# Kernel optimization log

Measured on AMD Instinct MI355X. Metric: run time of the kernel, lower is better.

## Reference

```python
import jax, jax.numpy as jnp
import numpy as np

N_QUBITS = 4
N_FEATURES = 16
B = 1048576


def _bcast(theta):
    # theta: scalar or [B]; make broadcastable against [B,2,2,2] amp slices
    return theta if jnp.ndim(theta) == 0 else theta.reshape(theta.shape[0], 1, 1, 1)


def apply_ry(state, theta, w):
    # state: [B,2,2,2,2] complex; RY(theta) on wire w
    th = _bcast(theta)
    c = jnp.cos(th / 2).astype(state.dtype)
    s = jnp.sin(th / 2).astype(state.dtype)
    st = jnp.moveaxis(state, w + 1, -1)
    a0, a1 = st[..., 0], st[..., 1]
    st = jnp.stack([c * a0 - s * a1, s * a0 + c * a1], axis=-1)
    return jnp.moveaxis(st, -1, w + 1)


def apply_rz(state, theta, w):
    # RZ(theta) = diag(e^{-i theta/2}, e^{+i theta/2}) on wire w
    th = _bcast(theta)
    ph = jnp.exp(-0.5j * th.astype(jnp.float32)).astype(state.dtype)
    st = jnp.moveaxis(state, w + 1, -1)
    a0, a1 = st[..., 0], st[..., 1]
    st = jnp.stack([ph * a0, jnp.conj(ph) * a1], axis=-1)
    return jnp.moveaxis(st, -1, w + 1)


def cnot(state, c, t):
    st = jnp.moveaxis(state, (c + 1, t + 1), (-2, -1))  # [...,2(ctrl),2(tgt)]
    st = jnp.stack([st[..., 0, :], st[..., 1, ::-1]], axis=-2)
    return jnp.moveaxis(st, (-2, -1), (c + 1, t + 1))


def quantum_encoder_batched(x, qw):
    # x: [B,16] float32, qw: [8] float32 -> latents [B,4] (PauliZ expvals)
    b = x.shape[0]
    state = jnp.zeros((b, 16), jnp.complex64).at[:, 0].set(1.0)
    state = state.reshape(b, 2, 2, 2, 2)
    pi = jnp.float32(np.pi)
    for i in range(N_QUBITS):
        state = apply_ry(state, x[:, i] * pi, i)
        state = apply_rz(state, x[:, i + N_QUBITS] * pi, i)
    for i in range(N_QUBITS - 1):
        state = cnot(state, i, i + 1)
    for i in range(N_QUBITS):
        state = apply_ry(state, qw[2 * i], i)
        state = apply_rz(state, qw[2 * i + 1], i)
    for i in range(N_QUBITS - 1):
        state = cnot(state, i, i + 1)
    probs = state.real ** 2 + state.imag ** 2  # [B,2,2,2,2]
    zs = []
    for i in range(N_QUBITS):
        axes = tuple(a for a in range(1, N_QUBITS + 1) if a != i + 1)
        p = probs.sum(axes)  # [B,2]
        zs.append(p[:, 0] - p[:, 1])
    return jnp.stack(zs, axis=1)  # [B,4]


def setup_inputs() -> dict:
    key = jax.random.key(0)
    ks = jax.random.split(key, 8)
    x = jax.random.uniform(ks[0], (B, N_FEATURES), dtype=jnp.float32)
    q_weights = 0.01 * jax.random.normal(ks[1], (2 * N_QUBITS,), dtype=jnp.float32)
    # decoder: Linear(4,16) -> ReLU -> Linear(16,32) -> ReLU -> Linear(32,16)
    W1 = jax.random.normal(ks[2], (16, 4), dtype=jnp.float32) / jnp.sqrt(4.0)
    b1 = jnp.zeros((16,), jnp.float32)
    W2 = jax.random.normal(ks[3], (32, 16), dtype=jnp.float32) / jnp.sqrt(16.0)
    b2 = jnp.zeros((32,), jnp.float32)
    W3 = jax.random.normal(ks[4], (16, 32), dtype=jnp.float32) / jnp.sqrt(32.0)
    b3 = jnp.zeros((16,), jnp.float32)
    return {"x": x, "q_weights": q_weights, "W1": W1, "b1": b1,
            "W2": W2, "b2": b2, "W3": W3, "b3": b3}


def reference(x, q_weights, W1, b1, W2, b2, W3, b3):
    z = quantum_encoder_batched(x, q_weights)          # [B,4]
    h = jax.nn.relu(z @ W1.T + b1)                      # [B,16]
    h = jax.nn.relu(h @ W2.T + b2)                      # [B,32]
    return h @ W3.T + b3                                # [B,16]
```

## Files before the change

kernel.cpp:

```cpp
#include <hip/hip_runtime.h>
#include <math.h>

using u32 = unsigned int;
typedef float v2f __attribute__((ext_vector_type(2)));

__device__ __forceinline__ v2f pkfma(v2f a, v2f b, v2f c) {
    return __builtin_elementwise_fma(a, b, c);
}
__device__ __forceinline__ v2f s2(float x) { return (v2f){x, x}; }

#define WS_FLOATS 1160

__global__ void cvt_weights_kernel(
    const float* __restrict__ qw, const float* __restrict__ W1, const float* __restrict__ b1,
    const float* __restrict__ W2, const float* __restrict__ b2, const float* __restrict__ W3,
    const float* __restrict__ b3, float* __restrict__ o)
{
    int t = blockIdx.x * blockDim.x + threadIdx.x;
    if (t >= WS_FLOATS) return;
    float v;
    if (t < 64) {
        int k = t >> 4, j = t & 15;
        v = W1[j * 4 + k];
    } else if (t < 80) {
        v = b1[t - 64];
    } else if (t < 592) {
        int idx = t - 80, k = idx >> 5, j = idx & 31;
        v = W2[j * 16 + k];
    } else if (t < 624) {
        v = b2[t - 592];
    } else if (t < 1136) {
        int idx = t - 624, k = idx >> 4, j = idx & 15;
        v = W3[j * 32 + k];
    } else if (t < 1152) {
        v = b3[t - 1136];
    } else if (t < 1156) {
        v = cosf(qw[2 * (t - 1152)] * 0.5f);
    } else {
        v = sinf(qw[2 * (t - 1156)] * 0.5f);
    }
    o[t] = v;
}

template<bool WS>
__global__ void __launch_bounds__(256) qae_main(
    const float* __restrict__ x,
    const float* __restrict__ wf,
    const float* __restrict__ qwp,
    const float* __restrict__ W1p, const float* __restrict__ b1p,
    const float* __restrict__ W2p, const float* __restrict__ b2p,
    const float* __restrict__ W3p, const float* __restrict__ b3p,
    float* __restrict__ outv, int n)
{
    int b = blockIdx.x * blockDim.x + threadIdx.x;
    if (b >= n) return;

    auto T1v = [&](int k, int j) -> v2f {
        if (WS) { int o = k * 16 + 2 * j; return (v2f){wf[o], wf[o + 1]}; }
        return (v2f){W1p[(2 * j) * 4 + k], W1p[(2 * j + 1) * 4 + k]};
    };
    auto T2v = [&](int k, int j) -> v2f {
        if (WS) { int o = 80 + k * 32 + 2 * j; return (v2f){wf[o], wf[o + 1]}; }
        return (v2f){W2p[(2 * j) * 16 + k], W2p[(2 * j + 1) * 16 + k]};
    };
    auto T3v = [&](int k, int j) -> v2f {
        if (WS) { int o = 624 + k * 16 + 2 * j; return (v2f){wf[o], wf[o + 1]}; }
        return (v2f){W3p[(2 * j) * 32 + k], W3p[(2 * j + 1) * 32 + k]};
    };
    auto B1v = [&](int j) -> v2f {
        if (WS) return (v2f){wf[64 + 2 * j], wf[64 + 2 * j + 1]};
        return (v2f){b1p[2 * j], b1p[2 * j + 1]};
    };
    auto B2v = [&](int j) -> v2f {
        if (WS) return (v2f){wf[592 + 2 * j], wf[592 + 2 * j + 1]};
        return (v2f){b2p[2 * j], b2p[2 * j + 1]};
    };
    auto B3v = [&](int j) -> v2f {
        if (WS) return (v2f){wf[1136 + 2 * j], wf[1136 + 2 * j + 1]};
        return (v2f){b3p[2 * j], b3p[2 * j + 1]};
    };

    const float4* xf = reinterpret_cast<const float4*>(x);
    float4 xa = xf[(size_t)b * 4];
    float4 xc = xf[(size_t)b * 4 + 1];
    float th[4] = { xa.x, xa.y, xa.z, xa.w };
    float ph[4] = { xc.x, xc.y, xc.z, xc.w };

    float u0r[4], u0i[4], u1r[4], u1i[4];
    #pragma unroll
    for (int i = 0; i < 4; ++i) {
        float ct = __builtin_amdgcn_cosf(th[i] * 0.25f);
        float st = __builtin_amdgcn_sinf(th[i] * 0.25f);
        float cp = __builtin_amdgcn_cosf(ph[i] * 0.25f);
        float sp = __builtin_amdgcn_sinf(ph[i] * 0.25f);
        u0r[i] = ct * cp;  u0i[i] = -ct * sp;
        u1r[i] = st * cp;  u1i[i] = st * sp;
    }

    float p01r[4], p01i[4], p23r[4], p23i[4];
    #pragma unroll
    for (int a = 0; a < 2; ++a) {
        #pragma unroll
        for (int c = 0; c < 2; ++c) {
            float arq = a ? u1r[0] : u0r[0], aiq = a ? u1i[0] : u0i[0];
            float brq = c ? u1r[1] : u0r[1], biq = c ? u1i[1] : u0i[1];
            p01r[a*2+c] = arq*brq - aiq*biq;
            p01i[a*2+c] = arq*biq + aiq*brq;
            float crq = a ? u1r[2] : u0r[2], ciq = a ? u1i[2] : u0i[2];
            float drq = c ? u1r[3] : u0r[3], diq = c ? u1i[3] : u0i[3];
            p23r[a*2+c] = crq*drq - ciq*diq;
            p23i[a*2+c] = crq*diq + ciq*drq;
        }
    }

    v2f amp[16];
    #pragma unroll
    for (int i = 0; i < 16; ++i) {
        int q0 = (i>>3)&1, q1 = (i>>2)&1, q2 = (i>>1)&1, q3 = i&1;
        int g = (q0<<3) | ((q1^q0)<<2) | ((q2^q1)<<1) | (q3^q2);
        int hi = g >> 2, lo = g & 3;
        amp[i] = (v2f){ p01r[hi]*p23r[lo] - p01i[hi]*p23i[lo],
                        p01r[hi]*p23i[lo] + p01i[hi]*p23r[lo] };
    }

    #pragma unroll
    for (int w = 0; w < 4; ++w) {
        float c, s;
        if (WS) { c = wf[1152 + w]; s = wf[1156 + w]; }
        else {
            const float INV4PI = 0.07957747154594767f;
            c = __builtin_amdgcn_cosf(qwp[2*w] * INV4PI);
            s = __builtin_amdgcn_sinf(qwp[2*w] * INV4PI);
        }
        v2f vc = s2(c), vs = s2(s);
        int stride = 1 << (3 - w);
        #pragma unroll
        for (int m = 0; m < 16; ++m) {
            if (m & stride) continue;
            int i0 = m, i1 = m | stride;
            v2f a0 = amp[i0], a1 = amp[i1];
            amp[i0] = pkfma(vc, a0, -(vs * a1));
            amp[i1] = pkfma(vc, a1,  (vs * a0));
        }
    }

    float p[16];
    #pragma unroll
    for (int i = 0; i < 16; ++i) {
        int q0 = (i>>3)&1, q1 = (i>>2)&1, q2 = (i>>1)&1, q3 = i&1;
        int g = (q0<<3) | ((q1^q0)<<2) | ((q2^q1)<<1) | (q3^q2);
        v2f q = amp[g] * amp[g];
        p[i] = q.x + q.y;
    }

    float s2a[8], s4[4];
    #pragma unroll
    for (int j = 0; j < 8; ++j) s2a[j] = p[2*j] + p[2*j+1];
    #pragma unroll
    for (int j = 0; j < 4; ++j) s4[j] = s2a[2*j] + s2a[2*j+1];
    float z0 = (s4[0] + s4[1]) - (s4[2] + s4[3]);
    float z1 = (s4[0] - s4[1]) + (s4[2] - s4[3]);
    float z2 = (s2a[0] - s2a[1]) + (s2a[2] - s2a[3]) + (s2a[4] - s2a[5]) + (s2a[6] - s2a[7]);
    float z3 = (p[0]-p[1]) + (p[2]-p[3]) + (p[4]-p[5]) + (p[6]-p[7])
             + (p[8]-p[9]) + (p[10]-p[11]) + (p[12]-p[13]) + (p[14]-p[15]);
    float zv[4] = { z0, z1, z2, z3 };

    const v2f vzero = s2(0.f);

    v2f acc1[8];
    #pragma unroll
    for (int j = 0; j < 8; ++j) acc1[j] = B1v(j);
    #pragma unroll
    for (int k = 0; k < 4; ++k) {
        v2f zk = s2(zv[k]);
        #pragma unroll
        for (int j = 0; j < 8; ++j) acc1[j] = pkfma(T1v(k, j), zk, acc1[j]);
    }
    float h1[16];
    #pragma unroll
    for (int j = 0; j < 8; ++j) {
        v2f r = __builtin_elementwise_max(acc1[j], vzero);
        h1[2*j] = r.x; h1[2*j+1] = r.y;
    }

    v2f acc2[16];
    #pragma unroll
    for (int j = 0; j < 16; ++j) acc2[j] = B2v(j);
    #pragma unroll
    for (int k = 0; k < 16; ++k) {
        v2f hk = s2(h1[k]);
        #pragma unroll
        for (int j = 0; j < 16; ++j) acc2[j] = pkfma(T2v(k, j), hk, acc2[j]);
    }
    float h2[32];
    #pragma unroll
    for (int j = 0; j < 16; ++j) {
        v2f r = __builtin_elementwise_max(acc2[j], vzero);
        h2[2*j] = r.x; h2[2*j+1] = r.y;
    }

    v2f acc3[8];
    #pragma unroll
    for (int j = 0; j < 8; ++j) acc3[j] = B3v(j);
    #pragma unroll
    for (int k = 0; k < 32; ++k) {
        v2f hk = s2(h2[k]);
        #pragma unroll
        for (int j = 0; j < 8; ++j) acc3[j] = pkfma(T3v(k, j), hk, acc3[j]);
    }

    float4* op = reinterpret_cast<float4*>(outv) + (size_t)b * 4;
    op[0] = make_float4(acc3[0].x, acc3[0].y, acc3[1].x, acc3[1].y);
    op[1] = make_float4(acc3[2].x, acc3[2].y, acc3[3].x, acc3[3].y);
    op[2] = make_float4(acc3[4].x, acc3[4].y, acc3[5].x, acc3[5].y);
    op[3] = make_float4(acc3[6].x, acc3[6].y, acc3[7].x, acc3[7].y);
}

extern "C" void kernel_launch(void* const* d_in, const int* in_sizes, int n_in,
                              void* d_out, int out_size, void* d_ws, size_t ws_size,
                              hipStream_t stream) {
    const float* x  = (const float*)d_in[0];
    const float* qw = (const float*)d_in[1];
    const float* W1 = (const float*)d_in[2];
    const float* b1 = (const float*)d_in[3];
    const float* W2 = (const float*)d_in[4];
    const float* b2 = (const float*)d_in[5];
    const float* W3 = (const float*)d_in[6];
    const float* b3 = (const float*)d_in[7];
    float* out = (float*)d_out;

    int n = in_sizes[0] / 16;
    int blocks = (n + 255) / 256;

    if (ws_size >= WS_FLOATS * sizeof(float)) {
        float* wf = (float*)d_ws;
        cvt_weights_kernel<<<5, 256, 0, stream>>>(qw, W1, b1, W2, b2, W3, b3, wf);
        qae_main<true><<<blocks, 256, 0, stream>>>(x, wf, qw, W1, b1, W2, b2, W3, b3,
                                                   out, n);
    } else {
        qae_main<false><<<blocks, 256, 0, stream>>>(x, nullptr, qw, W1, b1, W2, b2, W3, b3,
                                                    out, n);
    }
}
```

Baseline: 149.3 us.

## Run decoder MLP on MFMA bf16 with split-weight fragments in LDS

Replaces the per-thread packed-FMA decoder MLP with wave-level MFMA 16x16x32 bf16 matmuls. Weights are split into hi/lo bf16 pairs to keep near-fp32 accuracy on the weight side, while activations are staged through shared memory as bf16. The separate weight-conversion kernel is removed and each block builds its own weight fragments, which drops a launch. This cuts VALU FMA work but adds LDS traffic, several block barriers and a loss of precision from rounding activations to bf16.

```diff
diff --git a/kernel.cpp b/kernel.cpp
--- a/kernel.cpp
+++ b/kernel.cpp
@@ -1,91 +1,70 @@
 #include <hip/hip_runtime.h>
-#include <math.h>
-
+
+using u16 = unsigned short;
 using u32 = unsigned int;
-typedef float v2f __attribute__((ext_vector_type(2)));
-
-__device__ __forceinline__ v2f pkfma(v2f a, v2f b, v2f c) {
-    return __builtin_elementwise_fma(a, b, c);
+typedef float v2f   __attribute__((ext_vector_type(2)));
+typedef float f32x4 __attribute__((ext_vector_type(4)));
+typedef short s16x8 __attribute__((ext_vector_type(8)));
+
+__device__ __forceinline__ float bf2f(u32 b) { return __uint_as_float(b << 16); }
+__device__ __forceinline__ u32   f2bf(float f) {
+    u32 u = __float_as_uint(f);
+    return (u + 0x7FFFu + ((u >> 16) & 1u)) >> 16;
 }
-__device__ __forceinline__ v2f s2(float x) { return (v2f){x, x}; }
-
-#define WS_FLOATS 1160
-
-__global__ void cvt_weights_kernel(
-    const float* __restrict__ qw, const float* __restrict__ W1, const float* __restrict__ b1,
-    const float* __restrict__ W2, const float* __restrict__ b2, const float* __restrict__ W3,
-    const float* __restrict__ b3, float* __restrict__ o)
+__device__ __forceinline__ v2f pkfma(v2f a, v2f b, v2f c) { return __builtin_elementwise_fma(a, b, c); }
+__device__ __forceinline__ v2f s2v(float x) { return (v2f){x, x}; }
+
+__global__ void __launch_bounds__(256) qae_fused(
+    const float* __restrict__ x,  const float* __restrict__ qw,
+    const float* __restrict__ W1, const float* __restrict__ b1,
+    const float* __restrict__ W2, const float* __restrict__ b2,
+    const float* __restrict__ W3, const float* __restrict__ b3,
+    float* __restrict__ out, int n)
 {
-    int t = blockIdx.x * blockDim.x + threadIdx.x;
-    if (t >= WS_FLOATS) return;
-    float v;
-    if (t < 64) {
-        int k = t >> 4, j = t & 15;
-        v = W1[j * 4 + k];
-    } else if (t < 80) {
-        v = b1[t - 64];
-    } else if (t < 592) {
-        int idx = t - 80, k = idx >> 5, j = idx & 31;
-        v = W2[j * 16 + k];
-    } else if (t < 624) {
-        v = b2[t - 592];
-    } else if (t < 1136) {
-        int idx = t - 624, k = idx >> 4, j = idx & 15;
-        v = W3[j * 32 + k];
-    } else if (t < 1152) {
-        v = b3[t - 1136];
-    } else if (t < 1156) {
-        v = cosf(qw[2 * (t - 1152)] * 0.5f);
-    } else {
-        v = sinf(qw[2 * (t - 1156)] * 0.5f);
-    }
-    o[t] = v;
-}
-
-template<bool WS>
-__global__ void __launch_bounds__(256) qae_main(
-    const float* __restrict__ x,
-    const float* __restrict__ wf,
-    const float* __restrict__ qwp,
-    const float* __restrict__ W1p, const float* __restrict__ b1p,
-    const float* __restrict__ W2p, const float* __restrict__ b2p,
-    const float* __restrict__ W3p, const float* __restrict__ b3p,
-    float* __restrict__ outv, int n)
-{
-    int b = blockIdx.x * blockDim.x + threadIdx.x;
-    if (b >= n) return;
-
-    auto T1v = [&](int k, int j) -> v2f {
-        if (WS) { int o = k * 16 + 2 * j; return (v2f){wf[o], wf[o + 1]}; }
-        return (v2f){W1p[(2 * j) * 4 + k], W1p[(2 * j + 1) * 4 + k]};
-    };
-    auto T2v = [&](int k, int j) -> v2f {
-        if (WS) { int o = 80 + k * 32 + 2 * j; return (v2f){wf[o], wf[o + 1]}; }
-        return (v2f){W2p[(2 * j) * 16 + k], W2p[(2 * j + 1) * 16 + k]};
-    };
-    auto T3v = [&](int k, int j) -> v2f {
-        if (WS) { int o = 624 + k * 16 + 2 * j; return (v2f){wf[o], wf[o + 1]}; }
-        return (v2f){W3p[(2 * j) * 32 + k], W3p[(2 * j + 1) * 32 + k]};
-    };
-    auto B1v = [&](int j) -> v2f {
-        if (WS) return (v2f){wf[64 + 2 * j], wf[64 + 2 * j + 1]};
-        return (v2f){b1p[2 * j], b1p[2 * j + 1]};
-    };
-    auto B2v = [&](int j) -> v2f {
-        if (WS) return (v2f){wf[592 + 2 * j], wf[592 + 2 * j + 1]};
-        return (v2f){b2p[2 * j], b2p[2 * j + 1]};
-    };
-    auto B3v = [&](int j) -> v2f {
-        if (WS) return (v2f){wf[1136 + 2 * j], wf[1136 + 2 * j + 1]};
-        return (v2f){b3p[2 * j], b3p[2 * j + 1]};
-    };
+    int tid  = threadIdx.x;
+    int b    = blockIdx.x * 256 + tid;
+    int bc   = b < n ? b : n - 1;
+    int lane = tid & 63;
+    int quad = lane >> 4, col = lane & 15;
+    int wbase = (tid >> 6) * 64;
+
+    __shared__ union {
+        u16 frag[8 * 512];
+        struct { u16 Zb[256 * 4]; u16 H1[256 * 24]; u16 H2[256 * 36]; } m;
+    } sh;
 
     const float4* xf = reinterpret_cast<const float4*>(x);
-    float4 xa = xf[(size_t)b * 4];
-    float4 xc = xf[(size_t)b * 4 + 1];
+    float4 xa = xf[(size_t)bc * 4];
+    float4 xc = xf[(size_t)bc * 4 + 1];
+
+    #pragma unroll
+    for (int e = 0; e < 16; ++e) {
+        int t  = tid * 16 + e;
+        int f  = t >> 9, idx = t & 511;
+        int ln = idx >> 3, j = idx & 7;
+        int nn = ln & 15, qd = ln >> 4, k = qd * 8 + j;
+        int ff = f >> 1;
+        float w = 0.f; bool valid = false;
+        if      (ff == 0) { valid = (k < 4);  if (valid) w = W1[nn * 4 + k]; }
+        else if (ff == 1) { valid = (k < 16); if (valid) w = W2[nn * 16 + k]; }
+        else if (ff == 2) { valid = (k < 16); if (valid) w = W2[(16 + nn) * 16 + k]; }
+        else              { valid = true;               w = W3[nn * 32 + k]; }
+        u16 hb = (u16)f2bf(w);
+        u16 lb = (u16)f2bf(w - bf2f(hb));
+        sh.frag[t] = valid ? ((f & 1) ? lb : hb) : (u16)0;
+    }
+
+    const float INV4PI = 0.07957747154594767f;
+    float qc[4], qs[4];
+    #pragma unroll
+    for (int w = 0; w < 4; ++w) {
+        float a = qw[2 * w];
+        qc[w] = __builtin_amdgcn_cosf(a * INV4PI);
+        qs[w] = __builtin_amdgcn_sinf(a * INV4PI);
+    }
+
     float th[4] = { xa.x, xa.y, xa.z, xa.w };
     float ph[4] = { xc.x, xc.y, xc.z, xc.w };
-
     float u0r[4], u0i[4], u1r[4], u1i[4];
     #pragma unroll
     for (int i = 0; i < 4; ++i) {
@@ -96,10 +75,9 @@
         u0r[i] = ct * cp;  u0i[i] = -ct * sp;
         u1r[i] = st * cp;  u1i[i] = st * sp;
     }
-
     float p01r[4], p01i[4], p23r[4], p23i[4];
     #pragma unroll
-    for (int a = 0; a < 2; ++a) {
+    for (int a = 0; a < 2; ++a)
         #pragma unroll
         for (int c = 0; c < 2; ++c) {
             float arq = a ? u1r[0] : u0r[0], aiq = a ? u1i[0] : u0i[0];
@@ -111,28 +89,18 @@
             p23r[a*2+c] = crq*drq - ciq*diq;
             p23i[a*2+c] = crq*diq + ciq*drq;
         }
-    }
-
     v2f amp[16];
     #pragma unroll
     for (int i = 0; i < 16; ++i) {
-        int q0 = (i>>3)&1, q1 = (i>>2)&1, q2 = (i>>1)&1, q3 = i&1;
+        int q0=(i>>3)&1, q1=(i>>2)&1, q2=(i>>1)&1, q3=i&1;
         int g = (q0<<3) | ((q1^q0)<<2) | ((q2^q1)<<1) | (q3^q2);
         int hi = g >> 2, lo = g & 3;
         amp[i] = (v2f){ p01r[hi]*p23r[lo] - p01i[hi]*p23i[lo],
                         p01r[hi]*p23i[lo] + p01i[hi]*p23r[lo] };
     }
-
     #pragma unroll
     for (int w = 0; w < 4; ++w) {
-        float c, s;
-        if (WS) { c = wf[1152 + w]; s = wf[1156 + w]; }
-        else {
-            const float INV4PI = 0.07957747154594767f;
-            c = __builtin_amdgcn_cosf(qwp[2*w] * INV4PI);
-            s = __builtin_amdgcn_sinf(qwp[2*w] * INV4PI);
-        }
-        v2f vc = s2(c), vs = s2(s);
+        v2f vc = s2v(qc[w]), vs = s2v(qs[w]);
         int stride = 1 << (3 - w);
         #pragma unroll
         for (int m = 0; m < 16; ++m) {
@@ -143,77 +111,98 @@
             amp[i1] = pkfma(vc, a1,  (vs * a0));
         }
     }
-
     float p[16];
     #pragma unroll
     for (int i = 0; i < 16; ++i) {
-        int q0 = (i>>3)&1, q1 = (i>>2)&1, q2 = (i>>1)&1, q3 = i&1;
+        int q0=(i>>3)&1, q1=(i>>2)&1, q2=(i>>1)&1, q3=i&1;
         int g = (q0<<3) | ((q1^q0)<<2) | ((q2^q1)<<1) | (q3^q2);
         v2f q = amp[g] * amp[g];
         p[i] = q.x + q.y;
     }
-
     float s2a[8], s4[4];
     #pragma unroll
     for (int j = 0; j < 8; ++j) s2a[j] = p[2*j] + p[2*j+1];
     #pragma unroll
     for (int j = 0; j < 4; ++j) s4[j] = s2a[2*j] + s2a[2*j+1];
-    float z0 = (s4[0] + s4[1]) - (s4[2] + s4[3]);
-    float z1 = (s4[0] - s4[1]) + (s4[2] - s4[3]);
-    float z2 = (s2a[0] - s2a[1]) + (s2a[2] - s2a[3]) + (s2a[4] - s2a[5]) + (s2a[6] - s2a[7]);
-    float z3 = (p[0]-p[1]) + (p[2]-p[3]) + (p[4]-p[5]) + (p[6]-p[7])
-             + (p[8]-p[9]) + (p[10]-p[11]) + (p[12]-p[13]) + (p[14]-p[15]);
-    float zv[4] = { z0, z1, z2, z3 };
-
-    const v2f vzero = s2(0.f);
-
-    v2f acc1[8];
-    #pragma unroll
-    for (int j = 0; j < 8; ++j) acc1[j] = B1v(j);
-    #pragma unroll
-    for (int k = 0; k < 4; ++k) {
-        v2f zk = s2(zv[k]);
-        #pragma unroll
-        for (int j = 0; j < 8; ++j) acc1[j] = pkfma(T1v(k, j), zk, acc1[j]);
-    }
-    float h1[16];
-    #pragma unroll
-    for (int j = 0; j < 8; ++j) {
-        v2f r = __builtin_elementwise_max(acc1[j], vzero);
-        h1[2*j] = r.x; h1[2*j+1] = r.y;
-    }
-
-    v2f acc2[16];
-    #pragma unroll
-    for (int j = 0; j < 16; ++j) acc2[j] = B2v(j);
-    #pragma unroll
-    for (int k = 0; k < 16; ++k) {
-        v2f hk = s2(h1[k]);
-        #pragma unroll
-        for (int j = 0; j < 16; ++j) acc2[j] = pkfma(T2v(k, j), hk, acc2[j]);
-    }
-    float h2[32];
-    #pragma unroll
-    for (int j = 0; j < 16; ++j) {
-        v2f r = __builtin_elementwise_max(acc2[j], vzero);
-        h2[2*j] = r.x; h2[2*j+1] = r.y;
-    }
-
-    v2f acc3[8];
-    #pragma unroll
-    for (int j = 0; j < 8; ++j) acc3[j] = B3v(j);
-    #pragma unroll
-    for (int k = 0; k < 32; ++k) {
-        v2f hk = s2(h2[k]);
-        #pragma unroll
-        for (int j = 0; j < 8; ++j) acc3[j] = pkfma(T3v(k, j), hk, acc3[j]);
-    }
-
-    float4* op = reinterpret_cast<float4*>(outv) + (size_t)b * 4;
-    op[0] = make_float4(acc3[0].x, acc3[0].y, acc3[1].x, acc3[1].y);
-    op[1] = make_float4(acc3[2].x, acc3[2].y, acc3[3].x, acc3[3].y);
-    op[2] = make_float4(acc3[4].x, acc3[4].y, acc3[5].x, acc3[5].y);
-    op[3] = make_float4(acc3[6].x, acc3[6].y, acc3[7].x, acc3[7].y);
+    float zv[4];
+    zv[0] = (s4[0] + s4[1]) - (s4[2] + s4[3]);
+    zv[1] = (s4[0] - s4[1]) + (s4[2] - s4[3]);
+    zv[2] = (s2a[0]-s2a[1]) + (s2a[2]-s2a[3]) + (s2a[4]-s2a[5]) + (s2a[6]-s2a[7]);
+    zv[3] = (p[0]-p[1]) + (p[2]-p[3]) + (p[4]-p[5]) + (p[6]-p[7])
+          + (p[8]-p[9]) + (p[10]-p[11]) + (p[12]-p[13]) + (p[14]-p[15]);
+
+    __syncthreads();
+    union U { uint4 u; s16x8 s; };
+    s16x8 Bf[8];
+    #pragma unroll
+    for (int f = 0; f < 8; ++f) {
+        U cv; cv.u = *reinterpret_cast<const uint4*>(&sh.frag[f * 512 + lane * 8]);
+        Bf[f] = cv.s;
+    }
+    float b1v = b1[col], b2v0 = b2[col], b2v1 = b2[16 + col], b3v = b3[col];
+    __syncthreads();
+
+    u32 zlo = f2bf(zv[0]) | (f2bf(zv[1]) << 16);
+    u32 zhi = f2bf(zv[2]) | (f2bf(zv[3]) << 16);
+    *reinterpret_cast<uint2*>(&sh.m.Zb[tid * 4]) = make_uint2(zlo, zhi);
+    __syncthreads();
+
+    #pragma unroll
+    for (int t = 0; t < 4; ++t) {
+        int arow = wbase + t * 16 + col;
+        U av; av.u = make_uint4(0, 0, 0, 0);
+        if (quad == 0) {
+            uint2 z = *reinterpret_cast<const uint2*>(&sh.m.Zb[arow * 4]);
+            av.u.x = z.x; av.u.y = z.y;
+        }
+        f32x4 c = { b1v, b1v, b1v, b1v };
+        c = __builtin_amdgcn_mfma_f32_16x16x32_bf16(av.s, Bf[1], c, 0, 0, 0);
+        c = __builtin_amdgcn_mfma_f32_16x16x32_bf16(av.s, Bf[0], c, 0, 0, 0);
+        #pragma unroll
+        for (int r = 0; r < 4; ++r) {
+            int row = wbase + t * 16 + quad * 4 + r;
+            sh.m.H1[row * 24 + col] = (u16)f2bf(fmaxf(c[r], 0.f));
+        }
+    }
+    __syncthreads();
+
+    #pragma unroll
+    for (int t = 0; t < 4; ++t) {
+        int arow = wbase + t * 16 + col;
+        U av; av.u = make_uint4(0, 0, 0, 0);
+        if (quad < 2)
+            av.u = *reinterpret_cast<const uint4*>(&sh.m.H1[arow * 24 + quad * 8]);
+        #pragma unroll
+        for (int nt = 0; nt < 2; ++nt) {
+            float bv = nt ? b2v1 : b2v0;
+            f32x4 c = { bv, bv, bv, bv };
+            c = __builtin_amdgcn_mfma_f32_16x16x32_bf16(av.s, Bf[3 + 2*nt], c, 0, 0, 0);
+            c = __builtin_amdgcn_mfma_f32_16x16x32_bf16(av.s, Bf[2 + 2*nt], c, 0, 0, 0);
+            #pragma unroll
+            for (int r = 0; r < 4; ++r) {
+                int row = wbase + t * 16 + quad * 4 + r;
+                sh.m.H2[row * 36 + nt * 16 + col] = (u16)f2bf(fmaxf(c[r], 0.f));
+            }
+        }
+    }
+    __syncthreads();
+
+    #pragma unroll
+    for (int t = 0; t < 4; ++t) {
+        int arow = wbase + t * 16 + col;
+        uint2 u0 = *reinterpret_cast<const uint2*>(&sh.m.H2[arow * 36 + quad * 8]);
+        uint2 u1 = *reinterpret_cast<const uint2*>(&sh.m.H2[arow * 36 + quad * 8 + 4]);
+        U av; av.u = make_uint4(u0.x, u0.y, u1.x, u1.y);
+        f32x4 c = { b3v, b3v, b3v, b3v };
+        c = __builtin_amdgcn_mfma_f32_16x16x32_bf16(av.s, Bf[7], c, 0, 0, 0);
+        c = __builtin_amdgcn_mfma_f32_16x16x32_bf16(av.s, Bf[6], c, 0, 0, 0);
+        int rowbase = blockIdx.x * 256 + wbase + t * 16 + quad * 4;
+        #pragma unroll
+        for (int r = 0; r < 4; ++r) {
+            int grow = rowbase + r;
+            if (grow < n) out[(size_t)grow * 16 + col] = c[r];
+        }
+    }
 }
 
 extern "C" void kernel_launch(void* const* d_in, const int* in_sizes, int n_in,
@@ -231,14 +220,5 @@
 
     int n = in_sizes[0] / 16;
     int blocks = (n + 255) / 256;
-
-    if (ws_size >= WS_FLOATS * sizeof(float)) {
-        float* wf = (float*)d_ws;
-        cvt_weights_kernel<<<5, 256, 0, stream>>>(qw, W1, b1, W2, b2, W3, b3, wf);
-        qae_main<true><<<blocks, 256, 0, stream>>>(x, wf, qw, W1, b1, W2, b2, W3, b3,
-                                                   out, n);
-    } else {
-        qae_main<false><<<blocks, 256, 0, stream>>>(x, nullptr, qw, W1, b1, W2, b2, W3, b3,
-                                                    out, n);
-    }
+    qae_fused<<<blocks, 256, 0, stream>>>(x, qw, W1, b1, W2, b2, W3, b3, out, n);
 }
```

New measurement: 149.0 us. About the same (-0.2%).
